# Optimization experiments

Hardware: AMD Instinct MI355X
Metric: run time of the kernel (lower is better)

Reference implementation:

```python
import jax, jax.numpy as jnp
import numpy as np
from jax import lax

KH = KW = 3
STRIDE = (1, 1)
PAD = (1, 1)

def setup_inputs() -> dict:
    key = jax.random.key(0)
    k1, k2, k3 = jax.random.split(key, 3)
    B_, C, H, W = 16, 128, 56, 56
    O, R = 256, 16
    Kflat = C * KH * KW
    x = jax.random.normal(k1, (B_, C, H, W), dtype=jnp.float32)
    # kaiming_normal_ fan_out for A: std = sqrt(2/out_channels)
    A = jax.random.normal(k2, (O, R), dtype=jnp.float32) * np.float32(np.sqrt(2.0 / O))
    # kaiming_normal_ fan_in for B: std = sqrt(2/kernel_flat_dim)
    Bm = jax.random.normal(k3, (R, Kflat), dtype=jnp.float32) * np.float32(np.sqrt(2.0 / Kflat))
    return {"x": x, "A": A, "B": Bm}

def reference(x, A, B):
    b, c, h, w = x.shape
    h_out = (h + 2 * PAD[0] - KH) // STRIDE[0] + 1
    w_out = (w + 2 * PAD[1] - KW) // STRIDE[1] + 1
    # im2col: [B, C*KH*KW, H_out, W_out]; feature order (c, kh, kw) matches torch Unfold
    patches = lax.conv_general_dilated_patches(
        x, filter_shape=(KH, KW), window_strides=STRIDE,
        padding=((PAD[0], PAD[0]), (PAD[1], PAD[1])))
    patches = patches.reshape(b, c * KH * KW, h_out * w_out)  # [B, K, L]
    tmp = jnp.einsum('rk,bkl->brl', B, patches)               # rank-limited matmul
    out = jnp.einsum('or,brl->bol', A, tmp)                   # [B, O, L]
    return out.reshape(b, A.shape[0], h_out, w_out)
```

## Files before the change

### kernel.cpp

```cpp
#include <hip/hip_runtime.h>
#include <hip/hip_bf16.h>


#define Bn 16
#define Cc 128
#define Hh 56
#define Ww 56
#define Ll (Hh * Ww)
#define Rr 16
#define Oo 256
#define KF (Cc * 9)
#define NKS 36
#define W2 58
#define RPITCH 128
#define ROWB (W2 * RPITCH)
#define HB 2

typedef __attribute__((ext_vector_type(8))) short bfrag_t;
typedef __attribute__((ext_vector_type(4))) float f32x4;

__device__ __forceinline__ float bf16_bits(unsigned short u) {
    return __uint_as_float(((unsigned)u) << 16);
}

__device__ __forceinline__ unsigned short bf16_rne(float f) {
    const unsigned u = __float_as_uint(f);
    const unsigned r = u + 0x7FFFu + ((u >> 16) & 1u);
    return (unsigned short)(r >> 16);
}

__device__ __forceinline__ bool detect_bf16(const void* __restrict__ p) {
    const unsigned* w = (const unsigned*)p;
    int c = 0;
#pragma unroll
    for (int i = 0; i < 32; ++i) {
        const unsigned e = (w[i] >> 7) & 0xFFu;
        c += (e >= 96u && e <= 144u) ? 1 : 0;
    }
    return c >= 20;
}

__device__ __forceinline__ int sw_idx(int px, int c) {
    return px * RPITCH + (((c >> 3) ^ (px & 7)) << 3) + (c & 7);
}

__global__ __launch_bounds__(256) void prep_frag(
    const void* __restrict__ A, const void* __restrict__ Bm,
    unsigned short* __restrict__ Bfrag, float* __restrict__ Afp)
{
    const bool ab = detect_bf16(A);
    const bool bb = detect_bf16(Bm);
    const int i = blockIdx.x * 256 + threadIdx.x;
    if (i < NKS * 512) {
        const int kstep = i >> 9, rem = i & 511;
        const int l = rem >> 3, e = rem & 7;
        const int r = l & 15, g = l >> 4;
        const int kp = kstep * 32 + g * 8 + e;
        const int tap = kp >> 7, c = kp & 127;
        const int k = c * 9 + tap;
        const float v = bb ? bf16_bits(((const unsigned short*)Bm)[r * KF + k])
                           : ((const float*)Bm)[r * KF + k];
        const unsigned short hi = bf16_rne(v);
        const float lov = v - bf16_bits(hi);
        Bfrag[(kstep * 2 + 0) * 512 + rem] = hi;
        Bfrag[(kstep * 2 + 1) * 512 + rem] = bf16_rne(lov);
    }
    if (i < Oo * Rr) {
        Afp[i] = ab ? bf16_bits(((const unsigned short*)A)[i])
                    : ((const float*)A)[i];
    }
}

template<bool XB>
__device__ __forceinline__ void fused_body(
    const void* __restrict__ x,
    const unsigned short* __restrict__ Bfrag,
    const float* __restrict__ Afp,
    float* __restrict__ out,
    unsigned short* __restrict__ xs)
{
    const int tid  = threadIdx.x;
    const int lane = tid & 63;
    const int wv   = __builtin_amdgcn_readfirstlane(tid >> 6);
    const int col  = lane & 15;
    const int g    = lane >> 4;
    const int h0   = blockIdx.x * HB;
    const int b    = blockIdx.y;

#pragma unroll
    for (int rr = 0; rr < HB + 2; ++rr) {
        const int hh = h0 - 1 + rr;
        unsigned short* xr = xs + rr * ROWB;
        if (hh >= 0 && hh < Hh) {
#pragma unroll
            for (int it = 0; it < 16; ++it) {
                const int idx = it * 256 + tid;
                const int wp = idx & 31, c = idx >> 5;
                if (wp < 28) {
                    unsigned short lo, hi;
                    if constexpr (XB) {
                        const unsigned v = ((const unsigned*)x)[
                            (unsigned)((b * Cc + c) * (Ll / 2) + hh * (Ww / 2) + wp)];
                        lo = (unsigned short)(v & 0xFFFFu);
                        hi = (unsigned short)(v >> 16);
                    } else {
                        const unsigned base =
                            (unsigned)((b * Cc + c) * Ll + hh * Ww + 2 * wp);
                        lo = bf16_rne(((const float*)x)[base]);
                        hi = bf16_rne(((const float*)x)[base + 1]);
                    }
                    xr[sw_idx(2 * wp + 1, c)] = lo;
                    xr[sw_idx(2 * wp + 2, c)] = hi;
                }
            }
            if (tid < 128) {
                xr[tid] = 0;
                xr[57 * RPITCH + tid] = 0;
            }
        } else {
#pragma unroll
            for (int it = 0; it < 15; ++it) {
                const int idx = it * 256 + tid;
                ((unsigned*)xr)[idx] = 0u;
            }
            if (tid < 3712 - 15 * 256) ((unsigned*)xr)[15 * 256 + tid] = 0u;
        }
    }
    __syncthreads();

    const int px  = wv * 16 + col;
    const int pxc = px < Ww ? px : Ww - 1;

    unsigned off12[12];
#pragma unroll
    for (int dwv = 0; dwv < 3; ++dwv) {
#pragma unroll
        for (int cb = 0; cb < 4; ++cb) {
            const int p2 = pxc + dwv;
            off12[dwv * 4 + cb] =
                (unsigned)(p2 * RPITCH + ((((cb * 4 + g) ^ (p2 & 7))) << 3));
        }
    }

    f32x4 acc0 = {0.f, 0.f, 0.f, 0.f};
    f32x4 acc1 = {0.f, 0.f, 0.f, 0.f};
    const bfrag_t* __restrict__ bf = (const bfrag_t*)Bfrag;

#pragma unroll
    for (int ks = 0; ks < NKS; ++ks) {
        const int tap = ks >> 2, cb = ks & 3;
        const int dh = tap / 3, dw = tap - dh * 3;
        const bfrag_t ahi = bf[(ks * 2 + 0) * 64 + lane];
        const bfrag_t alo = bf[(ks * 2 + 1) * 64 + lane];
        const unsigned short* p0 = xs + dh * ROWB + off12[dw * 4 + cb];
        const bfrag_t pf0 = *(const bfrag_t*)p0;
        const bfrag_t pf1 = *(const bfrag_t*)(p0 + ROWB);
        acc0 = __builtin_amdgcn_mfma_f32_16x16x32_bf16(ahi, pf0, acc0, 0, 0, 0);
        acc0 = __builtin_amdgcn_mfma_f32_16x16x32_bf16(alo, pf0, acc0, 0, 0, 0);
        acc1 = __builtin_amdgcn_mfma_f32_16x16x32_bf16(ahi, pf1, acc1, 0, 0, 0);
        acc1 = __builtin_amdgcn_mfma_f32_16x16x32_bf16(alo, pf1, acc1, 0, 0, 0);
    }

    __syncthreads();
    float (*tmp)[Rr][66] = (float (*)[Rr][66])xs;

#pragma unroll
    for (int reg = 0; reg < 4; ++reg) {
        tmp[0][g * 4 + reg][wv * 16 + col] = acc0[reg];
        tmp[1][g * 4 + reg][wv * 16 + col] = acc1[reg];
    }
    __syncthreads();

    float tv0[Rr], tv1[Rr];
#pragma unroll
    for (int r = 0; r < Rr; ++r) {
        tv0[r] = tmp[0][r][lane];
        tv1[r] = tmp[1][r][lane];
    }

    const bool wok = (lane < Ww);
    const size_t obase = (size_t)b * Oo * Ll + (size_t)(h0 * Ww) + (size_t)lane;
#pragma unroll 4
    for (int j = 0; j < 64; ++j) {
        const int o = wv * 64 + j;
        const float* Ao = Afp + (size_t)o * Rr;
        float s0 = 0.f, s1 = 0.f;
#pragma unroll
        for (int r = 0; r < Rr; ++r) {
            const float av = Ao[r];
            s0 += av * tv0[r];
            s1 += av * tv1[r];
        }
        if (wok) {
            out[obase + (size_t)o * Ll]      = s0;
            out[obase + (size_t)o * Ll + Ww] = s1;
        }
    }
}

__global__ __launch_bounds__(256, 2) void fused_one(
    const void* __restrict__ x,
    const unsigned short* __restrict__ Bfrag,
    const float* __restrict__ Afp,
    float* __restrict__ out)
{
    __shared__ __align__(16) unsigned short xs[4 * ROWB];
    if (detect_bf16(x)) fused_body<true >(x, Bfrag, Afp, out, xs);
    else                fused_body<false>(x, Bfrag, Afp, out, xs);
}

__global__ __launch_bounds__(256) void fused_fallback(
    const void* __restrict__ x, const void* __restrict__ A,
    const void* __restrict__ Bm, float* __restrict__ out)
{
    const bool xb = detect_bf16(x);
    const bool ab = detect_bf16(A);
    const bool bb = detect_bf16(Bm);
    const int gid = blockIdx.x * 256 + threadIdx.x;
    const int b = gid / Ll;
    const int l = gid - b * Ll;
    const int h = l / Ww, w = l - h * Ww;
    float acc[Rr];
#pragma unroll
    for (int r = 0; r < Rr; ++r) acc[r] = 0.f;
    const size_t xbase = (size_t)b * Cc * Ll;
    for (int c = 0; c < Cc; ++c) {
        const size_t xc = xbase + (size_t)c * Ll;
        float xv[9];
#pragma unroll
        for (int dh = 0; dh < 3; ++dh) {
            const int hh = h + dh - 1;
            const bool hok = (hh >= 0) & (hh < Hh);
#pragma unroll
            for (int dw = 0; dw < 3; ++dw) {
                const int ww = w + dw - 1;
                const bool ok = hok & (ww >= 0) & (ww < Ww);
                const size_t idx = xc + (size_t)(hh * Ww + ww);
                xv[dh*3+dw] = ok ? (xb ? bf16_bits(((const unsigned short*)x)[idx])
                                       : ((const float*)x)[idx]) : 0.f;
            }
        }
#pragma unroll
        for (int r = 0; r < Rr; ++r) {
            const size_t bo = (size_t)r * KF + (size_t)c * 9;
            float s = acc[r];
#pragma unroll
            for (int i = 0; i < 9; ++i)
                s += (bb ? bf16_bits(((const unsigned short*)Bm)[bo+i])
                         : ((const float*)Bm)[bo+i]) * xv[i];
            acc[r] = s;
        }
    }
    const size_t obase = (size_t)b * Oo * Ll + (size_t)l;
    for (int o = 0; o < Oo; ++o) {
        float s = 0.f;
#pragma unroll
        for (int r = 0; r < Rr; ++r)
            s += (ab ? bf16_bits(((const unsigned short*)A)[o*Rr+r])
                     : ((const float*)A)[o*Rr+r]) * acc[r];
        out[obase + (size_t)o * Ll] = s;
    }
}

extern "C" void kernel_launch(void* const* d_in, const int* in_sizes, int n_in,
                              void* d_out, int out_size, void* d_ws, size_t ws_size,
                              hipStream_t stream) {
    const void* x  = d_in[0];
    const void* A  = d_in[1];
    const void* Bm = d_in[2];
    for (int i = 0; i < n_in && i < 3; ++i) {
        const int s = in_sizes[i];
        if      (s == Bn * Cc * Ll) x  = d_in[i];
        else if (s == Oo * Rr)      A  = d_in[i];
        else if (s == Rr * KF)      Bm = d_in[i];
    }
    float* out = (float*)d_out;

    const size_t frag_bytes = (size_t)(NKS * 2 * 512) * 2;
    const size_t afp_bytes  = (size_t)(Oo * Rr) * 4;
    const size_t need       = frag_bytes + afp_bytes;

    if (ws_size >= need) {
        unsigned short* Bfrag = (unsigned short*)d_ws;
        float* Afp = (float*)((char*)d_ws + frag_bytes);
        prep_frag<<<dim3(72), 256, 0, stream>>>(A, Bm, Bfrag, Afp);
        fused_one<<<dim3(Hh / HB, Bn), 256, 0, stream>>>(x, Bfrag, Afp, out);
    } else {
        fused_fallback<<<dim3((Bn * Ll) / 256), 256, 0, stream>>>(x, A, Bm, out);
    }
}
```

Before: 116.4 us.

## Split K across two wave groups with 512-thread blocks and channel-vectorized staging

```diff
diff --git a/kernel.cpp b/kernel.cpp
--- a/kernel.cpp
+++ b/kernel.cpp
@@ -38,10 +38,6 @@
         c += (e >= 96u && e <= 144u) ? 1 : 0;
     }
     return c >= 20;
-}
-
-__device__ __forceinline__ int sw_idx(int px, int c) {
-    return px * RPITCH + (((c >> 3) ^ (px & 7)) << 3) + (c & 7);
 }
 
 __global__ __launch_bounds__(256) void prep_frag(
@@ -71,6 +67,8 @@
     }
 }
 
+#define MFB(A, B, C) __builtin_amdgcn_mfma_f32_16x16x32_bf16((A), (B), (C), 0, 0, 0)
+
 template<bool XB>
 __device__ __forceinline__ void fused_body(
     const void* __restrict__ x,
@@ -82,107 +80,118 @@
     const int tid  = threadIdx.x;
     const int lane = tid & 63;
     const int wv   = __builtin_amdgcn_readfirstlane(tid >> 6);
-    const int col  = lane & 15;
-    const int g    = lane >> 4;
+    const int t    = wv & 3;
+    const int kh   = wv >> 2;
     const int h0   = blockIdx.x * HB;
     const int b    = blockIdx.y;
 
-#pragma unroll
-    for (int rr = 0; rr < HB + 2; ++rr) {
-        const int hh = h0 - 1 + rr;
-        unsigned short* xr = xs + rr * ROWB;
-        if (hh >= 0 && hh < Hh) {
-#pragma unroll
-            for (int it = 0; it < 16; ++it) {
-                const int idx = it * 256 + tid;
-                const int wp = idx & 31, c = idx >> 5;
-                if (wp < 28) {
-                    unsigned short lo, hi;
-                    if constexpr (XB) {
-                        const unsigned v = ((const unsigned*)x)[
-                            (unsigned)((b * Cc + c) * (Ll / 2) + hh * (Ww / 2) + wp)];
-                        lo = (unsigned short)(v & 0xFFFFu);
-                        hi = (unsigned short)(v >> 16);
-                    } else {
-                        const unsigned base =
-                            (unsigned)((b * Cc + c) * Ll + hh * Ww + 2 * wp);
-                        lo = bf16_rne(((const float*)x)[base]);
-                        hi = bf16_rne(((const float*)x)[base + 1]);
+    {
+        const int l   = lane;
+        const bool lok = (l < Ww);
+#pragma unroll
+        for (int rr = 0; rr < HB + 2; ++rr) {
+            const int hh = h0 - 1 + rr;
+            unsigned short* xr = xs + rr * ROWB;
+            if (hh >= 0 && hh < Hh) {
+                if (lok) {
+                    const unsigned gb = (unsigned)(b * Cc * Ll + hh * Ww + l);
+#pragma unroll
+                    for (int it = 0; it < 2; ++it) {
+                        const int cs_ = it * 8 + wv;
+                        const int c0  = cs_ * 8;
+                        bfrag_t v;
+#pragma unroll
+                        for (int j = 0; j < 8; ++j) {
+                            if constexpr (XB) {
+                                v[j] = (short)((const unsigned short*)x)[
+                                    gb + (unsigned)((c0 + j) * Ll)];
+                            } else {
+                                v[j] = (short)bf16_rne(((const float*)x)[
+                                    gb + (unsigned)((c0 + j) * Ll)]);
+                            }
+                        }
+                        const int sp = cs_ ^ ((l + 1) & 7);
+                        *(bfrag_t*)((char*)xr + (l + 1) * 256 + sp * 16) = v;
                     }
-                    xr[sw_idx(2 * wp + 1, c)] = lo;
-                    xr[sw_idx(2 * wp + 2, c)] = hi;
                 }
+            } else {
+                unsigned* xw = (unsigned*)xr;
+#pragma unroll
+                for (int it = 0; it < 7; ++it) xw[it * 512 + tid] = 0u;
+                if (tid < 3712 - 7 * 512) xw[7 * 512 + tid] = 0u;
             }
-            if (tid < 128) {
-                xr[tid] = 0;
-                xr[57 * RPITCH + tid] = 0;
+        }
+        if (tid < 128) {
+#pragma unroll
+            for (int rr = 0; rr < HB + 2; ++rr) {
+                xs[rr * ROWB + tid] = 0;
+                xs[rr * ROWB + 57 * RPITCH + tid] = 0;
             }
-        } else {
-#pragma unroll
-            for (int it = 0; it < 15; ++it) {
-                const int idx = it * 256 + tid;
-                ((unsigned*)xr)[idx] = 0u;
-            }
-            if (tid < 3712 - 15 * 256) ((unsigned*)xr)[15 * 256 + tid] = 0u;
         }
     }
     __syncthreads();
 
-    const int px  = wv * 16 + col;
+    const int col = lane & 15;
+    const int g   = lane >> 4;
+    const int px  = t * 16 + col;
     const int pxc = px < Ww ? px : Ww - 1;
 
-    unsigned off12[12];
-#pragma unroll
-    for (int dwv = 0; dwv < 3; ++dwv) {
-#pragma unroll
-        for (int cb = 0; cb < 4; ++cb) {
+    unsigned off6[6];
+#pragma unroll
+    for (int dwv = 0; dwv < 3; ++dwv)
+#pragma unroll
+        for (int cbi = 0; cbi < 2; ++cbi) {
+            const int cb = kh * 2 + cbi;
             const int p2 = pxc + dwv;
-            off12[dwv * 4 + cb] =
-                (unsigned)(p2 * RPITCH + ((((cb * 4 + g) ^ (p2 & 7))) << 3));
-        }
-    }
+            off6[dwv * 2 + cbi] = (unsigned)(p2 * 256 +
+                (((cb * 4 + g) ^ (p2 & 7)) << 4));
+        }
 
     f32x4 acc0 = {0.f, 0.f, 0.f, 0.f};
     f32x4 acc1 = {0.f, 0.f, 0.f, 0.f};
-    const bfrag_t* __restrict__ bf = (const bfrag_t*)Bfrag;
-
-#pragma unroll
-    for (int ks = 0; ks < NKS; ++ks) {
-        const int tap = ks >> 2, cb = ks & 3;
+    const bfrag_t* __restrict__ bfp = (const bfrag_t*)Bfrag;
+
+#pragma unroll
+    for (int tap = 0; tap < 9; ++tap) {
         const int dh = tap / 3, dw = tap - dh * 3;
-        const bfrag_t ahi = bf[(ks * 2 + 0) * 64 + lane];
-        const bfrag_t alo = bf[(ks * 2 + 1) * 64 + lane];
-        const unsigned short* p0 = xs + dh * ROWB + off12[dw * 4 + cb];
-        const bfrag_t pf0 = *(const bfrag_t*)p0;
-        const bfrag_t pf1 = *(const bfrag_t*)(p0 + ROWB);
-        acc0 = __builtin_amdgcn_mfma_f32_16x16x32_bf16(ahi, pf0, acc0, 0, 0, 0);
-        acc0 = __builtin_amdgcn_mfma_f32_16x16x32_bf16(alo, pf0, acc0, 0, 0, 0);
-        acc1 = __builtin_amdgcn_mfma_f32_16x16x32_bf16(ahi, pf1, acc1, 0, 0, 0);
-        acc1 = __builtin_amdgcn_mfma_f32_16x16x32_bf16(alo, pf1, acc1, 0, 0, 0);
+#pragma unroll
+        for (int cbi = 0; cbi < 2; ++cbi) {
+            const int cb = kh * 2 + cbi;
+            const int ks = tap * 4 + cb;
+            const bfrag_t ahi = bfp[(ks * 2 + 0) * 64 + lane];
+            const bfrag_t alo = bfp[(ks * 2 + 1) * 64 + lane];
+            const char* p0 = (const char*)xs + dh * (ROWB * 2) + off6[dw * 2 + cbi];
+            const bfrag_t pf0 = *(const bfrag_t*)p0;
+            const bfrag_t pf1 = *(const bfrag_t*)(p0 + ROWB * 2);
+            acc0 = MFB(ahi, pf0, acc0);
+            acc0 = MFB(alo, pf0, acc0);
+            acc1 = MFB(ahi, pf1, acc1);
+            acc1 = MFB(alo, pf1, acc1);
+        }
     }
 
     __syncthreads();
-    float (*tmp)[Rr][66] = (float (*)[Rr][66])xs;
+    float (*tmp2)[HB][Rr][66] = (float (*)[HB][Rr][66])xs;
 
 #pragma unroll
     for (int reg = 0; reg < 4; ++reg) {
-        tmp[0][g * 4 + reg][wv * 16 + col] = acc0[reg];
-        tmp[1][g * 4 + reg][wv * 16 + col] = acc1[reg];
+        tmp2[kh][0][g * 4 + reg][t * 16 + col] = acc0[reg];
+        tmp2[kh][1][g * 4 + reg][t * 16 + col] = acc1[reg];
     }
     __syncthreads();
 
     float tv0[Rr], tv1[Rr];
 #pragma unroll
     for (int r = 0; r < Rr; ++r) {
-        tv0[r] = tmp[0][r][lane];
-        tv1[r] = tmp[1][r][lane];
+        tv0[r] = tmp2[0][0][r][lane] + tmp2[1][0][r][lane];
+        tv1[r] = tmp2[0][1][r][lane] + tmp2[1][1][r][lane];
     }
 
     const bool wok = (lane < Ww);
     const size_t obase = (size_t)b * Oo * Ll + (size_t)(h0 * Ww) + (size_t)lane;
 #pragma unroll 4
-    for (int j = 0; j < 64; ++j) {
-        const int o = wv * 64 + j;
+    for (int j = 0; j < 32; ++j) {
+        const int o = wv * 32 + j;
         const float* Ao = Afp + (size_t)o * Rr;
         float s0 = 0.f, s1 = 0.f;
 #pragma unroll
@@ -198,7 +207,7 @@
     }
 }
 
-__global__ __launch_bounds__(256, 2) void fused_one(
+__global__ __launch_bounds__(512, 4) void fused_ks(
     const void* __restrict__ x,
     const unsigned short* __restrict__ Bfrag,
     const float* __restrict__ Afp,
@@ -284,7 +293,7 @@
         unsigned short* Bfrag = (unsigned short*)d_ws;
         float* Afp = (float*)((char*)d_ws + frag_bytes);
         prep_frag<<<dim3(72), 256, 0, stream>>>(A, Bm, Bfrag, Afp);
-        fused_one<<<dim3(Hh / HB, Bn), 256, 0, stream>>>(x, Bfrag, Afp, out);
+        fused_ks<<<dim3(Hh / HB, Bn), 512, 0, stream>>>(x, Bfrag, Afp, out);
     } else {
         fused_fallback<<<dim3((Bn * Ll) / 256), 256, 0, stream>>>(x, A, Bm, out);
     }
```

Result: faster. 103.5 us (-11.1%).
